# Performance work log

Measured on AMD Instinct MI355X. Metric: run time of the kernel, lower is better.

Reference implementation:

```python
import jax, jax.numpy as jnp
import numpy as np

IN_SIZE = 171
HIDDEN = 1024
OUT_SIZE = 171
BATCH = 64
SEQ_LEN = 100
COND_NUM = 5
GT_NUM = 5


def _lstm_cell(x, h, c, w_ih, w_hh, b_ih, b_hh):
    # PyTorch LSTMCell: gates ordered (i, f, g, o)
    gates = x @ w_ih.T + h @ w_hh.T + b_ih + b_hh  # [B, 4H]
    i, f, g, o = jnp.split(gates, 4, axis=-1)
    i = jax.nn.sigmoid(i)
    f = jax.nn.sigmoid(f)
    g = jnp.tanh(g)
    o = jax.nn.sigmoid(o)
    c_new = f * c + i * g
    h_new = o * jnp.tanh(c_new)
    return h_new, c_new


def setup_inputs() -> dict:
    key = jax.random.key(0)
    ks = jax.random.split(key, 15)
    s = 1.0 / np.sqrt(HIDDEN)
    p = {}
    p["real_seq"] = jax.random.normal(ks[0], (BATCH, SEQ_LEN, IN_SIZE), dtype=jnp.float32)
    p["w_ih1"] = jax.random.uniform(ks[1], (4 * HIDDEN, IN_SIZE), minval=-s, maxval=s, dtype=jnp.float32)
    p["w_hh1"] = jax.random.uniform(ks[2], (4 * HIDDEN, HIDDEN), minval=-s, maxval=s, dtype=jnp.float32)
    p["b_ih1"] = jax.random.uniform(ks[3], (4 * HIDDEN,), minval=-s, maxval=s, dtype=jnp.float32)
    p["b_hh1"] = jax.random.uniform(ks[4], (4 * HIDDEN,), minval=-s, maxval=s, dtype=jnp.float32)
    p["w_ih2"] = jax.random.uniform(ks[5], (4 * HIDDEN, HIDDEN), minval=-s, maxval=s, dtype=jnp.float32)
    p["w_hh2"] = jax.random.uniform(ks[6], (4 * HIDDEN, HIDDEN), minval=-s, maxval=s, dtype=jnp.float32)
    p["b_ih2"] = jax.random.uniform(ks[7], (4 * HIDDEN,), minval=-s, maxval=s, dtype=jnp.float32)
    p["b_hh2"] = jax.random.uniform(ks[8], (4 * HIDDEN,), minval=-s, maxval=s, dtype=jnp.float32)
    p["w_ih3"] = jax.random.uniform(ks[9], (4 * HIDDEN, HIDDEN), minval=-s, maxval=s, dtype=jnp.float32)
    p["w_hh3"] = jax.random.uniform(ks[10], (4 * HIDDEN, HIDDEN), minval=-s, maxval=s, dtype=jnp.float32)
    p["b_ih3"] = jax.random.uniform(ks[11], (4 * HIDDEN,), minval=-s, maxval=s, dtype=jnp.float32)
    p["b_hh3"] = jax.random.uniform(ks[12], (4 * HIDDEN,), minval=-s, maxval=s, dtype=jnp.float32)
    p["dec_w"] = jax.random.uniform(ks[13], (OUT_SIZE, HIDDEN), minval=-s, maxval=s, dtype=jnp.float32)
    p["dec_b"] = jax.random.uniform(ks[14], (OUT_SIZE,), minval=-s, maxval=s, dtype=jnp.float32)
    return p


def _condition_lst(seq_len):
    gt = np.ones((100, GT_NUM))
    cond = np.zeros((100, COND_NUM))
    return np.concatenate((gt, cond), axis=1).reshape(-1)[:seq_len]


def reference(real_seq, w_ih1, w_hh1, b_ih1, b_hh1, w_ih2, w_hh2, b_ih2, b_hh2,
              w_ih3, w_hh3, b_ih3, b_hh3, dec_w, dec_b):
    batch, seq_len, _ = real_seq.shape
    cond = jnp.asarray(_condition_lst(seq_len), dtype=real_seq.dtype)  # [T], static pattern
    frames = jnp.swapaxes(real_seq, 0, 1)  # [T, B, in]
    z = jnp.zeros((batch, HIDDEN), dtype=real_seq.dtype)
    out0 = jnp.zeros((batch, OUT_SIZE), dtype=real_seq.dtype)

    def step(carry, xs):
        (h0, c0, h1, c1, h2, c2, prev_out) = carry
        frame, c = xs
        in_frame = jnp.where(c == 1, frame, prev_out)
        h0, c0 = _lstm_cell(in_frame, h0, c0, w_ih1, w_hh1, b_ih1, b_hh1)
        h1, c1 = _lstm_cell(h0, h1, c1, w_ih2, w_hh2, b_ih2, b_hh2)
        h2, c2 = _lstm_cell(h1, h2, c2, w_ih3, w_hh3, b_ih3, b_hh3)
        out = h2 @ dec_w.T + dec_b
        return (h0, c0, h1, c1, h2, c2, out), out

    _, outs = jax.lax.scan(step, (z, z, z, z, z, z, out0), (frames, cond))  # outs [T, B, out]
    # torch concatenates along dim=1 -> [B, T*out]
    return jnp.swapaxes(outs, 0, 1).reshape(batch, seq_len * OUT_SIZE)
```

## Files before the change

kernel.cpp:

```cpp
#include <hip/hip_runtime.h>
#include <hip/hip_fp16.h>


typedef unsigned short u16;
typedef unsigned int u32;
typedef _Float16 f16;
typedef _Float16 h8 __attribute__((ext_vector_type(8)));
typedef float f4 __attribute__((ext_vector_type(4)));

#define HSZ 65536

static __device__ __forceinline__ f4 mfma16(h8 a, h8 b, f4 c) {
  return __builtin_amdgcn_mfma_f32_16x16x32_f16(a, b, c, 0, 0, 0);
}

static __device__ __forceinline__ float fsig(float x) {
  return 1.f / (1.f + __expf(-x));
}
static __device__ __forceinline__ float ftanh(float x) {
  return 1.f - 2.f / (1.f + __expf(2.f * x));
}

struct P {
  const u16 *w1h, *weff, *w1x, *w2, *w3, *wdec, *fr;
  const float *br, *ba, *b2s, *b3s, *dec_b;
  u16 *h0, *h1, *h2;
  float* out;
  u32* bar;
};

template<int NJ>
static __device__ __forceinline__ void gemm_hreg(f4* acc, const u16* __restrict__ h,
                                                 const h8 (&wr)[NJ], int kq, int bt2,
                                                 int q, int c) {
#pragma unroll
  for (int jj = 0; jj < NJ; ++jj) {
    int kt = kq * 8 + jj;
    const u16* hp = h + (size_t)(kt * 4 + q) * 512;
    h8 b = wr[jj];
#pragma unroll
    for (int t = 0; t < 2; ++t) {
      h8 a = *(const h8*)(hp + ((bt2 * 2 + t) * 16 + c) * 8);
      acc[t] = mfma16(a, b, acc[t]);
    }
  }
}

static __device__ __forceinline__ void gemm_hlds(f4* acc, const u16* __restrict__ h,
                                                 const u16* lw, int ktbase, int kq,
                                                 int bt2, int q, int c, int lane) {
#pragma unroll
  for (int jj = 0; jj < 8; ++jj) {
    int kt = kq * 8 + jj;
    h8 b = *(const h8*)(lw + (size_t)((ktbase + kt) * 64 + lane) * 8);
    const u16* hp = h + (size_t)(kt * 4 + q) * 512;
#pragma unroll
    for (int t = 0; t < 2; ++t) {
      h8 a = *(const h8*)(hp + ((bt2 * 2 + t) * 16 + c) * 8);
      acc[t] = mfma16(a, b, acc[t]);
    }
  }
}

static __device__ __forceinline__ void gemm_fr(f4* acc, const u16* __restrict__ frt,
                                               const h8 (&wr)[2], int kq, int bt2,
                                               int q, int c) {
  if (kq < 3) {
#pragma unroll
    for (int jj = 0; jj < 2; ++jj) {
      int kt = kq * 2 + jj;
      h8 b = wr[jj];
#pragma unroll
      for (int t = 0; t < 2; ++t) {
        h8 a = *(const h8*)(frt + (size_t)((bt2 * 2 + t) * 16 + c) * 192 + kt * 32 + q * 8);
        acc[t] = mfma16(a, b, acc[t]);
      }
    }
  }
}

__launch_bounds__(512, 2)
__global__ void lstm_main(P p) {
  const int ng = blockIdx.x;
  const int tid = threadIdx.x;
  const int lane = tid & 63;
  const int w = tid >> 6;
  const int kq = w & 3;
  const int bt2 = w >> 2;
  const int c = lane & 15;
  const int q = lane >> 4;

  __shared__ u16 lds_w2[64 * 512];
  __shared__ u16 lds_w3[64 * 512];
  __shared__ float part[4 * 64 * 17];
  __shared__ float decp[8][64];

  {
    const uint4* s2 = (const uint4*)(p.w2 + (size_t)ng * 64 * 512);
    const uint4* s3 = (const uint4*)(p.w3 + (size_t)ng * 64 * 512);
    uint4* d2 = (uint4*)lds_w2;
    uint4* d3 = (uint4*)lds_w3;
    for (int i = tid; i < 4096; i += 512) { d2[i] = s2[i]; d3[i] = s3[i]; }
  }

  h8 r_w1h[8], r_weff[8], r_w1x[2];
  {
#pragma unroll
    for (int jj = 0; jj < 8; ++jj) {
      r_w1h[jj] = *(const h8*)(p.w1h + (size_t)((ng * 32 + kq * 8 + jj) * 64 + lane) * 8);
      r_weff[jj] = *(const h8*)(p.weff + (size_t)((ng * 32 + kq * 8 + jj) * 64 + lane) * 8);
    }
    if (kq < 3) {
#pragma unroll
      for (int jj = 0; jj < 2; ++jj)
        r_w1x[jj] = *(const h8*)(p.w1x + (size_t)((ng * 6 + kq * 2 + jj) * 64 + lane) * 8);
    }
  }

  float rb_r[16], rb_a[16], rb2[16], rb3[16];
  if (w == 0) {
#pragma unroll
    for (int i = 0; i < 16; ++i) {
      int idx = (i >> 2) * 1024 + ng * 4 + (i & 3);
      rb_r[i] = p.br[idx];  rb_a[i] = p.ba[idx];
      rb2[i] = p.b2s[idx];  rb3[i] = p.b3s[idx];
    }
  }
  const float dec_bng = (ng < 171) ? p.dec_b[ng] : 0.f;
  __syncthreads();

  float cr0[4] = {0, 0, 0, 0}, cr1[4] = {0, 0, 0, 0}, cr2[4] = {0, 0, 0, 0};
  u32 pub = 0;

  auto combine_pub = [&](float* crL, const float* rb, u16* hw) {
    u32 pk0 = 0, pk1 = 0;
#pragma unroll
    for (int u = 0; u < 4; ++u) {
      float s0 = rb[0 + u], s1 = rb[4 + u], s2 = rb[8 + u], s3 = rb[12 + u];
#pragma unroll
      for (int kqi = 0; kqi < 4; ++kqi) {
        const float* pp = &part[(kqi * 64 + lane) * 17 + u];
        s0 += pp[0]; s1 += pp[4]; s2 += pp[8]; s3 += pp[12];
      }
      float iv = fsig(s0), fv = fsig(s1), gv = ftanh(s2), ov = fsig(s3);
      float cn = fv * crL[u] + iv * gv;
      crL[u] = cn;
      f16 hh = (f16)(ov * ftanh(cn));
      u32 bits = (u32)*(const u16*)&hh;
      if (u < 2) pk0 |= bits << (16 * u); else pk1 |= bits << (16 * (u - 2));
    }
    u32* dst = (u32*)hw + (size_t)(ng >> 1) * 256 + lane * 4 + (ng & 1) * 2;
    __hip_atomic_store(dst, pk0, __ATOMIC_RELAXED, __HIP_MEMORY_SCOPE_AGENT);
    __hip_atomic_store(dst + 1, pk1, __ATOMIC_RELAXED, __HIP_MEMORY_SCOPE_AGENT);
    __builtin_amdgcn_s_waitcnt(0x0f70);
    if (lane == 0)
      __hip_atomic_store(p.bar + ng, pub, __ATOMIC_RELAXED, __HIP_MEMORY_SCOPE_AGENT);
  };

  auto waitall = [&]() {
    if (w == 0) {
      for (;;) {
        u32 v0 = __hip_atomic_load(p.bar + lane, __ATOMIC_RELAXED, __HIP_MEMORY_SCOPE_AGENT);
        u32 v1 = __hip_atomic_load(p.bar + 64 + lane, __ATOMIC_RELAXED, __HIP_MEMORY_SCOPE_AGENT);
        u32 v2 = __hip_atomic_load(p.bar + 128 + lane, __ATOMIC_RELAXED, __HIP_MEMORY_SCOPE_AGENT);
        u32 v3 = __hip_atomic_load(p.bar + 192 + lane, __ATOMIC_RELAXED, __HIP_MEMORY_SCOPE_AGENT);
        u32 m01 = v0 < v1 ? v0 : v1;
        u32 m23 = v2 < v3 ? v2 : v3;
        u32 mn = m01 < m23 ? m01 : m23;
        if (__all((int)(mn >= pub))) break;
      }
    }
    __syncthreads();
  };

  auto put_part = [&](const f4* acc) {
#pragma unroll
    for (int t = 0; t < 2; ++t)
#pragma unroll
      for (int r = 0; r < 4; ++r)
        part[(kq * 64 + bt2 * 32 + t * 16 + q * 4 + r) * 17 + c] = acc[t][r];
  };

  auto dec_partial = [&](const u16* __restrict__ h2b) {
    if (ng < 171) {
      const u16* hp = h2b + (size_t)w * 16 * 512 + lane * 8;
      const u16* wp = p.wdec + (size_t)ng * 1024 + w * 128;
      float s = 0.f;
#pragma unroll 4
      for (int i = 0; i < 16; ++i) {
        h8 hv = *(const h8*)(hp + (size_t)i * 512);
        h8 wv8 = *(const h8*)(wp + i * 8);
#pragma unroll
        for (int jj = 0; jj < 8; ++jj) s += (float)hv[jj] * (float)wv8[jj];
      }
      decp[w][lane] = s;
    }
  };
  auto dec_reduce = [&](int tout) {
    if (ng < 171) {
      float o = dec_bng;
#pragma unroll
      for (int i = 0; i < 8; ++i) o += decp[i][lane];
      p.out[(size_t)lane * 17100 + (size_t)tout * 171 + ng] = o;
    }
  };

  for (int t = 0; t < 100; ++t) {
    const bool cond = (t % 10) < 5;
    const u16* h0r = p.h0 + (size_t)t * HSZ;
    const u16* h1r = p.h1 + (size_t)t * HSZ;
    const u16* h2r = p.h2 + (size_t)t * HSZ;
    u16* h0w = p.h0 + (size_t)(t + 1) * HSZ;
    u16* h1w = p.h1 + (size_t)(t + 1) * HSZ;
    u16* h2w = p.h2 + (size_t)(t + 1) * HSZ;

    {
      f4 acc[2] = {{0, 0, 0, 0}, {0, 0, 0, 0}};
      gemm_hreg<8>(acc, h0r, r_w1h, kq, bt2, q, c);
      if (cond) {
        gemm_fr(acc, p.fr + (size_t)t * 64 * 192, r_w1x, kq, bt2, q, c);
        __syncthreads();
      } else {
        waitall();
        gemm_hreg<8>(acc, h2r, r_weff, kq, bt2, q, c);
      }
      put_part(acc);
      __syncthreads();
      ++pub;
      if (w == 0) combine_pub(cr0, cond ? rb_r : rb_a, h0w);
    }
    {
      f4 acc[2] = {{0, 0, 0, 0}, {0, 0, 0, 0}};
      gemm_hlds(acc, h1r, lds_w2, 32, kq, bt2, q, c, lane);
      waitall();
      gemm_hlds(acc, h0w, lds_w2, 0, kq, bt2, q, c, lane);
      put_part(acc);
      __syncthreads();
      ++pub;
      if (w == 0) combine_pub(cr1, rb2, h1w);
    }
    {
      f4 acc[2] = {{0, 0, 0, 0}, {0, 0, 0, 0}};
      gemm_hlds(acc, h2r, lds_w3, 32, kq, bt2, q, c, lane);
      if (t > 0) dec_partial(h2r);
      waitall();
      gemm_hlds(acc, h1w, lds_w3, 0, kq, bt2, q, c, lane);
      put_part(acc);
      __syncthreads();
      ++pub;
      if (w == 0) combine_pub(cr2, rb3, h2w);
      else if (w == 1 && t > 0) dec_reduce(t - 1);
    }
  }
  waitall();
  dec_partial(p.h2 + (size_t)100 * HSZ);
  __syncthreads();
  if (w == 0) dec_reduce(99);
}


__global__ void pack_w_kernel(const float* __restrict__ srcA, int KA,
                              const float* __restrict__ srcB, int KB,
                              u16* __restrict__ dst, int nkt) {
  int blk = blockIdx.x;
  int ng = blk / nkt, kt = blk % nkt;
  int lane = threadIdx.x;
  int c = lane & 15, q = lane >> 4;
  int row = (c >> 2) * 1024 + ng * 4 + (c & 3);
  int k0 = kt * 32 + q * 8;
  alignas(16) u16 outv[8];
  for (int j = 0; j < 8; ++j) {
    int k = k0 + j;
    float v = 0.f;
    if (k < KA) v = srcA[(size_t)row * KA + k];
    else if (k - KA < KB) v = srcB[(size_t)row * KB + (k - KA)];
    f16 hv = (f16)v;
    outv[j] = *(u16*)&hv;
  }
  *(uint4*)(dst + ((size_t)blk * 64 + lane) * 8) = *(const uint4*)outv;
}

__global__ void pack_weff_kernel(const float* __restrict__ w_ih1,
                                 const float* __restrict__ dec_w, u16* __restrict__ dst) {
  int blk = blockIdx.x;
  int ng = blk >> 5, kt = blk & 31;
  int lane = threadIdx.x;
  int c = lane & 15, q = lane >> 4;
  int row = (c >> 2) * 1024 + ng * 4 + (c & 3);
  int k0 = kt * 32 + q * 8;
  float acc[8] = {0.f, 0.f, 0.f, 0.f, 0.f, 0.f, 0.f, 0.f};
  for (int r = 0; r < 171; ++r) {
    float wi = w_ih1[(size_t)row * 171 + r];
    const float* dw = dec_w + (size_t)r * 1024 + k0;
#pragma unroll
    for (int j = 0; j < 8; ++j) acc[j] += wi * dw[j];
  }
  alignas(16) u16 outv[8];
  for (int j = 0; j < 8; ++j) { f16 hv = (f16)acc[j]; outv[j] = *(u16*)&hv; }
  *(uint4*)(dst + ((size_t)blk * 64 + lane) * 8) = *(const uint4*)outv;
}

__global__ void prep_bias_kernel(const float* b_ih1, const float* b_hh1,
                                 const float* w_ih1, const float* dec_b,
                                 const float* b_ih2, const float* b_hh2,
                                 const float* b_ih3, const float* b_hh3,
                                 float* br, float* ba, float* b2, float* b3) {
  int n = blockIdx.x * 256 + threadIdx.x;
  float s = b_ih1[n] + b_hh1[n];
  br[n] = s;
  float a = 0.f;
  for (int r = 0; r < 171; ++r) a += w_ih1[(size_t)n * 171 + r] * dec_b[r];
  ba[n] = s + a;
  b2[n] = b_ih2[n] + b_hh2[n];
  b3[n] = b_ih3[n] + b_hh3[n];
}

__global__ void pack_frames_kernel(const float* __restrict__ rs, u16* __restrict__ fr) {
  int i = blockIdx.x * 256 + threadIdx.x;
  int j = i % 192;
  int tb = i / 192;
  int b = tb % 64, t = tb / 64;
  float v = (j < 171) ? rs[((size_t)b * 100 + t) * 171 + j] : 0.f;
  f16 hv = (f16)v;
  fr[i] = *(u16*)&hv;
}

__global__ void pack_wdec_kernel(const float* __restrict__ dw, u16* __restrict__ dst) {
  int i = blockIdx.x * 256 + threadIdx.x;
  if (i < 171 * 1024) { f16 hv = (f16)dw[i]; dst[i] = *(u16*)&hv; }
}

__global__ void zero_kernel(u32* h0, u32* h1, u32* h2, u32* bar) {
  int i = blockIdx.x * 256 + threadIdx.x;
  h0[i] = 0; h1[i] = 0; h2[i] = 0;
  if (blockIdx.x < 8) bar[i] = 0;
}

extern "C" void kernel_launch(void* const* d_in, const int* in_sizes, int n_in,
                              void* d_out, int out_size, void* d_ws, size_t ws_size,
                              hipStream_t stream) {
  const float* real_seq = (const float*)d_in[0];
  const float* w_ih1 = (const float*)d_in[1];
  const float* w_hh1 = (const float*)d_in[2];
  const float* b_ih1 = (const float*)d_in[3];
  const float* b_hh1 = (const float*)d_in[4];
  const float* w_ih2 = (const float*)d_in[5];
  const float* w_hh2 = (const float*)d_in[6];
  const float* b_ih2 = (const float*)d_in[7];
  const float* b_hh2 = (const float*)d_in[8];
  const float* w_ih3 = (const float*)d_in[9];
  const float* w_hh3 = (const float*)d_in[10];
  const float* b_ih3 = (const float*)d_in[11];
  const float* b_hh3 = (const float*)d_in[12];
  const float* dec_w = (const float*)d_in[13];
  const float* dec_b = (const float*)d_in[14];

  char* ws = (char*)d_ws;
  size_t off = 0;
  auto alloc = [&](size_t bytes) {
    char* pp = ws + off;
    off += (bytes + 255) & ~(size_t)255;
    return pp;
  };
  u16* w1h  = (u16*)alloc(256ULL * 32 * 512 * 2);
  u16* weff = (u16*)alloc(256ULL * 32 * 512 * 2);
  u16* w1x  = (u16*)alloc(256ULL * 6 * 512 * 2);
  u16* w2   = (u16*)alloc(256ULL * 64 * 512 * 2);
  u16* w3   = (u16*)alloc(256ULL * 64 * 512 * 2);
  u16* wdec = (u16*)alloc(171ULL * 1024 * 2);
  u16* fr   = (u16*)alloc(100ULL * 64 * 192 * 2);
  u16* h0   = (u16*)alloc(101ULL * HSZ * 2);
  u16* h1   = (u16*)alloc(101ULL * HSZ * 2);
  u16* h2   = (u16*)alloc(101ULL * HSZ * 2);
  float* br  = (float*)alloc(4096 * 4);
  float* ba  = (float*)alloc(4096 * 4);
  float* b2s = (float*)alloc(4096 * 4);
  float* b3s = (float*)alloc(4096 * 4);
  u32* bar   = (u32*)alloc(8192);
  (void)ws_size; (void)in_sizes; (void)n_in; (void)out_size;

  pack_w_kernel<<<256 * 32, 64, 0, stream>>>(w_hh1, 1024, nullptr, 0, w1h, 32);
  pack_w_kernel<<<256 * 6, 64, 0, stream>>>(w_ih1, 171, nullptr, 0, w1x, 6);
  pack_w_kernel<<<256 * 64, 64, 0, stream>>>(w_ih2, 1024, w_hh2, 1024, w2, 64);
  pack_w_kernel<<<256 * 64, 64, 0, stream>>>(w_ih3, 1024, w_hh3, 1024, w3, 64);
  pack_weff_kernel<<<256 * 32, 64, 0, stream>>>(w_ih1, dec_w, weff);
  pack_wdec_kernel<<<(171 * 1024 + 255) / 256, 256, 0, stream>>>(dec_w, wdec);
  pack_frames_kernel<<<100 * 64 * 192 / 256, 256, 0, stream>>>(real_seq, fr);
  prep_bias_kernel<<<16, 256, 0, stream>>>(b_ih1, b_hh1, w_ih1, dec_b,
                                           b_ih2, b_hh2, b_ih3, b_hh3, br, ba, b2s, b3s);
  zero_kernel<<<128, 256, 0, stream>>>((u32*)h0, (u32*)h1, (u32*)h2, bar);

  P p{w1h, weff, w1x, w2, w3, wdec, fr, br, ba, b2s, b3s, dec_b,
      h0, h1, h2, (float*)d_out, bar};
  lstm_main<<<256, 512, 0, stream>>>(p);
}
```

Before: 2.026 ms.

## Use sentinel-filled hidden-state slots for data-driven readiness with cache-bypass stores

All hidden-state history slots except the first are now pre-filled with a sentinel value. Consumers check each loaded vector for the sentinel and re-poll with cache-bypassing loads until real data arrives, so readiness is detected from the data itself. Producers store their packed halves with system-coherent global stores and no longer wait on store completion before writing the flag. The flag poll is also widened to a single dwordx4 load per lane. The intent is to remove store-wait latency on the critical path of each step. In exchange, every hidden-state load gets a compare and vote, the init kernel must write the full history buffers, and correctness relies on the sentinel never being a valid fp16 pair and on store ordering.

Result: slower. 2.810 ms (+38.7%).

```diff
diff --git a/kernel.cpp b/kernel.cpp
--- a/kernel.cpp
+++ b/kernel.cpp
@@ -7,8 +7,11 @@
 typedef _Float16 f16;
 typedef _Float16 h8 __attribute__((ext_vector_type(8)));
 typedef float f4 __attribute__((ext_vector_type(4)));
+typedef u32 u32x4 __attribute__((ext_vector_type(4)));
+typedef u32 u32x2 __attribute__((ext_vector_type(2)));
 
 #define HSZ 65536
+#define SENT 0xFFFFFFFFu
 
 static __device__ __forceinline__ f4 mfma16(h8 a, h8 b, f4 c) {
   return __builtin_amdgcn_mfma_f32_16x16x32_f16(a, b, c, 0, 0, 0);
@@ -19,6 +22,23 @@
 }
 static __device__ __forceinline__ float ftanh(float x) {
   return 1.f - 2.f / (1.f + __expf(2.f * x));
+}
+
+static __device__ __forceinline__ h8 load_h8v(const u16* hp) {
+  union { u32x4 u; h8 h; } cv;
+  cv.u = *(const u32x4*)hp;
+  int bad = (cv.u.x == SENT) | (cv.u.y == SENT) | (cv.u.z == SENT) | (cv.u.w == SENT);
+  if (__builtin_expect(__any(bad), 0)) {
+    do {
+      u32x4 v;
+      asm volatile("global_load_dwordx4 %0, %1, off sc0 sc1"
+                   : "=v"(v) : "v"(hp) : "memory");
+      __builtin_amdgcn_s_waitcnt(0x0f70);
+      cv.u = v;
+      bad = (cv.u.x == SENT) | (cv.u.y == SENT) | (cv.u.z == SENT) | (cv.u.w == SENT);
+    } while (__any(bad));
+  }
+  return cv.h;
 }
 
 struct P {
@@ -40,7 +60,7 @@
     h8 b = wr[jj];
 #pragma unroll
     for (int t = 0; t < 2; ++t) {
-      h8 a = *(const h8*)(hp + ((bt2 * 2 + t) * 16 + c) * 8);
+      h8 a = load_h8v(hp + ((bt2 * 2 + t) * 16 + c) * 8);
       acc[t] = mfma16(a, b, acc[t]);
     }
   }
@@ -56,7 +76,7 @@
     const u16* hp = h + (size_t)(kt * 4 + q) * 512;
 #pragma unroll
     for (int t = 0; t < 2; ++t) {
-      h8 a = *(const h8*)(hp + ((bt2 * 2 + t) * 16 + c) * 8);
+      h8 a = load_h8v(hp + ((bt2 * 2 + t) * 16 + c) * 8);
       acc[t] = mfma16(a, b, acc[t]);
     }
   }
@@ -150,22 +170,26 @@
       if (u < 2) pk0 |= bits << (16 * u); else pk1 |= bits << (16 * (u - 2));
     }
     u32* dst = (u32*)hw + (size_t)(ng >> 1) * 256 + lane * 4 + (ng & 1) * 2;
-    __hip_atomic_store(dst, pk0, __ATOMIC_RELAXED, __HIP_MEMORY_SCOPE_AGENT);
-    __hip_atomic_store(dst + 1, pk1, __ATOMIC_RELAXED, __HIP_MEMORY_SCOPE_AGENT);
-    __builtin_amdgcn_s_waitcnt(0x0f70);
-    if (lane == 0)
-      __hip_atomic_store(p.bar + ng, pub, __ATOMIC_RELAXED, __HIP_MEMORY_SCOPE_AGENT);
+    u32x2 pk; pk.x = pk0; pk.y = pk1;
+    asm volatile("global_store_dwordx2 %0, %1, off sc0 sc1"
+                 : : "v"(dst), "v"(pk) : "memory");
+    if (lane == 0) {
+      u32* fl = p.bar + ng;
+      asm volatile("global_store_dword %0, %1, off sc0 sc1"
+                   : : "v"(fl), "v"(pub) : "memory");
+    }
   };
 
   auto waitall = [&]() {
     if (w == 0) {
+      const u32* fp = p.bar + lane * 4;
       for (;;) {
-        u32 v0 = __hip_atomic_load(p.bar + lane, __ATOMIC_RELAXED, __HIP_MEMORY_SCOPE_AGENT);
-        u32 v1 = __hip_atomic_load(p.bar + 64 + lane, __ATOMIC_RELAXED, __HIP_MEMORY_SCOPE_AGENT);
-        u32 v2 = __hip_atomic_load(p.bar + 128 + lane, __ATOMIC_RELAXED, __HIP_MEMORY_SCOPE_AGENT);
-        u32 v3 = __hip_atomic_load(p.bar + 192 + lane, __ATOMIC_RELAXED, __HIP_MEMORY_SCOPE_AGENT);
-        u32 m01 = v0 < v1 ? v0 : v1;
-        u32 m23 = v2 < v3 ? v2 : v3;
+        u32x4 v;
+        asm volatile("global_load_dwordx4 %0, %1, off sc0 sc1"
+                     : "=v"(v) : "v"(fp) : "memory");
+        __builtin_amdgcn_s_waitcnt(0x0f70);
+        u32 m01 = v.x < v.y ? v.x : v.y;
+        u32 m23 = v.z < v.w ? v.z : v.w;
         u32 mn = m01 < m23 ? m01 : m23;
         if (__all((int)(mn >= pub))) break;
       }
@@ -188,7 +212,7 @@
       float s = 0.f;
 #pragma unroll 4
       for (int i = 0; i < 16; ++i) {
-        h8 hv = *(const h8*)(hp + (size_t)i * 512);
+        h8 hv = load_h8v(hp + (size_t)i * 512);
         h8 wv8 = *(const h8*)(wp + i * 8);
 #pragma unroll
         for (int jj = 0; jj < 8; ++jj) s += (float)hv[jj] * (float)wv8[jj];
@@ -330,10 +354,12 @@
   if (i < 171 * 1024) { f16 hv = (f16)dw[i]; dst[i] = *(u16*)&hv; }
 }
 
-__global__ void zero_kernel(u32* h0, u32* h1, u32* h2, u32* bar) {
+__global__ void init_kernel(u32* h0, u32* h1, u32* h2, u32* bar) {
   int i = blockIdx.x * 256 + threadIdx.x;
-  h0[i] = 0; h1[i] = 0; h2[i] = 0;
-  if (blockIdx.x < 8) bar[i] = 0;
+  const int SLOT = 32768;
+  u32 v = (i < SLOT) ? 0u : SENT;
+  h0[i] = v; h1[i] = v; h2[i] = v;
+  if (i < 2048) bar[i] = 0;
 }
 
 extern "C" void kernel_launch(void* const* d_in, const int* in_sizes, int n_in,
@@ -388,7 +414,7 @@
   pack_frames_kernel<<<100 * 64 * 192 / 256, 256, 0, stream>>>(real_seq, fr);
   prep_bias_kernel<<<16, 256, 0, stream>>>(b_ih1, b_hh1, w_ih1, dec_b,
                                            b_ih2, b_hh2, b_ih3, b_hh3, br, ba, b2s, b3s);
-  zero_kernel<<<128, 256, 0, stream>>>((u32*)h0, (u32*)h1, (u32*)h2, bar);
+  init_kernel<<<101 * 32768 / 256, 256, 0, stream>>>((u32*)h0, (u32*)h1, (u32*)h2, bar);
 
   P p{w1h, weff, w1x, w2, w3, wdec, fr, br, ba, b2s, b3s, dec_b,
       h0, h1, h2, (float*)d_out, bar};
```
